# Optimization experiments

Measured on AMD Instinct MI355X. Metric: run time of the kernel, lower is better.

The kernel has to match this reference:

```python
import jax, jax.numpy as jnp
import numpy as np
import math

HID, NH, NKV, HD = 2048, 16, 4, 128
GROUPS = NH // NKV
ROPE_THETA = 10000.0
NBITS = 8


def fake_quant(x, n_bits=NBITS):
    """Per-tensor symmetric min-max fake quantization with STE."""
    qmax = float(2 ** (n_bits - 1) - 1)
    scale = jnp.maximum(jnp.max(jnp.abs(x)) / qmax, jnp.asarray(1e-8, x.dtype))
    q = jnp.clip(jnp.round(x / scale), -qmax - 1.0, qmax) * scale
    return x + jax.lax.stop_gradient(q - x)


def quant_linear(x, w):
    # QuantLinear: fake-quant activation and weight, then x @ w.T
    return jnp.einsum('bsh,oh->bso', fake_quant(x), fake_quant(w))


def rope_cos_sin(position_ids, head_dim, dtype):
    inv_freq = 1.0 / (ROPE_THETA ** (jnp.arange(0, head_dim, 2, dtype=jnp.float32) / head_dim))
    freqs = position_ids.astype(jnp.float32)[..., None] * inv_freq  # [B,S,hd/2]
    emb = jnp.concatenate([freqs, freqs], axis=-1)                   # [B,S,hd]
    return jnp.cos(emb).astype(dtype), jnp.sin(emb).astype(dtype)


def rotate_half(x):
    h = x.shape[-1] // 2
    return jnp.concatenate([-x[..., h:], x[..., :h]], axis=-1)


def setup_inputs() -> dict:
    key = jax.random.key(0)
    ks = jax.random.split(key, 6)
    B, S = 2, 2048
    hidden_states = jax.random.normal(ks[0], (B, S, HID), dtype=jnp.float32)
    neg = jnp.finfo(jnp.float32).min
    causal = jnp.where(jnp.tril(jnp.ones((S, S), dtype=bool)), 0.0, neg).astype(jnp.float32)
    attention_mask = jnp.broadcast_to(causal[None, None], (B, 1, S, S))
    position_ids = jnp.broadcast_to(jnp.arange(S, dtype=jnp.int64)[None], (B, S))
    wq = jax.random.normal(ks[1], (NH * HD, HID), dtype=jnp.float32) * 0.02
    wk = jax.random.normal(ks[2], (NKV * HD, HID), dtype=jnp.float32) * 0.02
    wv = jax.random.normal(ks[3], (NKV * HD, HID), dtype=jnp.float32) * 0.02
    wo = jax.random.normal(ks[4], (HID, NH * HD), dtype=jnp.float32) * 0.02
    return {"hidden_states": hidden_states, "attention_mask": attention_mask,
            "position_ids": position_ids, "wq": wq, "wk": wk, "wv": wv, "wo": wo}


def reference(hidden_states, attention_mask, position_ids, wq, wk, wv, wo):
    B, S, _ = hidden_states.shape
    dtype = hidden_states.dtype
    # quantized projections -> [B, nH, S, hd] / [B, nKV, S, hd]
    q = quant_linear(hidden_states, wq).reshape(B, S, NH, HD).transpose(0, 2, 1, 3)
    k = quant_linear(hidden_states, wk).reshape(B, S, NKV, HD).transpose(0, 2, 1, 3)
    v = quant_linear(hidden_states, wv).reshape(B, S, NKV, HD).transpose(0, 2, 1, 3)
    # RoPE
    cos, sin = rope_cos_sin(position_ids, HD, dtype)
    cos, sin = cos[:, None], sin[:, None]  # broadcast over heads
    q = q * cos + rotate_half(q) * sin
    k = k * cos + rotate_half(k) * sin
    # repeat_kv (GQA)
    k = jnp.repeat(k, GROUPS, axis=1)
    v = jnp.repeat(v, GROUPS, axis=1)
    # fake-quantized QK^T
    q = fake_quant(q)
    k = fake_quant(k)
    attn_weights = jnp.einsum('bhqd,bhkd->bhqk', q, k) / math.sqrt(HD)
    attn_weights = attn_weights + attention_mask
    attn_weights = jnp.maximum(attn_weights, jnp.finfo(attn_weights.dtype).min)
    attn_weights = jax.nn.softmax(attn_weights.astype(jnp.float32), axis=-1).astype(dtype)
    # fake-quantized PV
    p = fake_quant(attn_weights)
    v = fake_quant(v)
    attn_output = jnp.einsum('bhqk,bhkd->bhqd', p, v)
    attn_output = attn_output.transpose(0, 2, 1, 3).reshape(B, S, NH * HD)
    return quant_linear(attn_output, wo)
```

## Files before the change

### kernel.cpp

```cpp
#include <hip/hip_runtime.h>
#include <math.h>
#include <stdint.h>
#include <stddef.h>

#define HID 2048
#define NH 16
#define NKV 4
#define HD 128
#define GROUPS (NH / NKV)
#define BATCH 2
#define SEQ 2048

#define N_HS  8388608ull
#define N_Q   8388608ull
#define N_KV  2097152ull
#define N_WQ  4194304ull
#define N_WKV 1048576ull
#define N_WO  4194304ull

typedef __attribute__((ext_vector_type(8))) short bf16x8;
typedef __attribute__((ext_vector_type(4))) float f32x4;

#define LOG2E 1.4426950408889634f
#define CLAMP_L2 115.41560325f

__device__ inline float quantv(float x, float s) {
  float q = rintf(x / s);
  return fminf(fmaxf(q, -128.0f), 127.0f);
}

__device__ inline float slot_scale(const unsigned int* slots, int i) {
  return fmaxf(__uint_as_float(slots[i]) / 127.0f, 1e-8f);
}

__device__ inline unsigned short f2bf(float x) {
  return (unsigned short)(__float_as_uint(x) >> 16);
}

__device__ inline float amax4(float4 v) {
  return fmaxf(fmaxf(fabsf(v.x), fabsf(v.y)), fmaxf(fabsf(v.z), fabsf(v.w)));
}

__device__ inline void block_amax_atomic(float m, unsigned int* slot) {
  __shared__ float red[256];
  red[threadIdx.x] = m;
  __syncthreads();
  for (int o = 128; o > 0; o >>= 1) {
    if (threadIdx.x < o) red[threadIdx.x] = fmaxf(red[threadIdx.x], red[threadIdx.x + o]);
    __syncthreads();
  }
  if (threadIdx.x == 0) atomicMax(slot, __float_as_uint(red[0]));
}

__device__ __forceinline__ void gload_lds16(const void* g, void* l) {
  __builtin_amdgcn_global_load_lds((const __attribute__((address_space(1))) unsigned int*)g,
                                   (__attribute__((address_space(3))) unsigned int*)l, 16, 0, 0);
}

__global__ __launch_bounds__(256) void absmax5_k(const float* __restrict__ a0,
                                                 const float* __restrict__ a1,
                                                 const float* __restrict__ a2,
                                                 const float* __restrict__ a3,
                                                 const float* __restrict__ a4,
                                                 unsigned int* __restrict__ slots) {
  const int t = blockIdx.y;
  const float* x = t == 0 ? a0 : t == 1 ? a1 : t == 2 ? a2 : t == 3 ? a3 : a4;
  const size_t n4 = (t == 0 ? N_HS : t == 1 ? N_WQ : t == 2 ? N_WKV : t == 3 ? N_WKV : N_WO) / 4;
  const float4* xp = (const float4*)x;
  float m = 0.0f;
  for (size_t i = (size_t)blockIdx.x * 256 + threadIdx.x; i < n4; i += (size_t)gridDim.x * 256)
    m = fmaxf(m, amax4(xp[i]));
  block_amax_atomic(m, slots + t);
}

__global__ __launch_bounds__(256) void quant5_k(const float* __restrict__ a0,
                                                const float* __restrict__ a1,
                                                const float* __restrict__ a2,
                                                const float* __restrict__ a3,
                                                const float* __restrict__ a4,
                                                const unsigned int* __restrict__ slots,
                                                unsigned short* __restrict__ o0,
                                                unsigned short* __restrict__ o1,
                                                unsigned short* __restrict__ o2,
                                                unsigned short* __restrict__ o3,
                                                unsigned short* __restrict__ o4) {
  const int t = blockIdx.y;
  const float* x = t == 0 ? a0 : t == 1 ? a1 : t == 2 ? a2 : t == 3 ? a3 : a4;
  unsigned short* o = t == 0 ? o0 : t == 1 ? o1 : t == 2 ? o2 : t == 3 ? o3 : o4;
  const size_t n4 = (t == 0 ? N_HS : t == 1 ? N_WQ : t == 2 ? N_WKV : t == 3 ? N_WKV : N_WO) / 4;
  const float s = fmaxf(__uint_as_float(slots[t]) / 127.0f, 1e-8f);
  const float4* xp = (const float4*)x;
  ushort4* op = (ushort4*)o;
  for (size_t i = (size_t)blockIdx.x * 256 + threadIdx.x; i < n4; i += (size_t)gridDim.x * 256) {
    float4 v = xp[i];
    ushort4 r;
    r.x = f2bf(quantv(v.x, s));
    r.y = f2bf(quantv(v.y, s));
    r.z = f2bf(quantv(v.z, s));
    r.w = f2bf(quantv(v.w, s));
    op[i] = r;
  }
}

__global__ __launch_bounds__(256) void quant2_k(const float* __restrict__ a0,
                                                const float* __restrict__ a1,
                                                const unsigned int* __restrict__ slots,
                                                unsigned short* __restrict__ o0,
                                                unsigned short* __restrict__ o1) {
  const int t = blockIdx.y;
  const float* x = t == 0 ? a0 : a1;
  unsigned short* o = t == 0 ? o0 : o1;
  const size_t n4 = (t == 0 ? N_Q : N_KV) / 4;
  const float s = fmaxf(__uint_as_float(slots[5 + t]) / 127.0f, 1e-8f);
  const float4* xp = (const float4*)x;
  ushort4* op = (ushort4*)o;
  for (size_t i = (size_t)blockIdx.x * 256 + threadIdx.x; i < n4; i += (size_t)gridDim.x * 256) {
    float4 v = xp[i];
    ushort4 r;
    r.x = f2bf(quantv(v.x, s));
    r.y = f2bf(quantv(v.y, s));
    r.z = f2bf(quantv(v.z, s));
    r.w = f2bf(quantv(v.w, s));
    op[i] = r;
  }
}

__global__ __launch_bounds__(256) void quant1_k(const float* __restrict__ x, size_t n4,
                                                const unsigned int* __restrict__ slot,
                                                unsigned short* __restrict__ out) {
  const float s = fmaxf(__uint_as_float(*slot) / 127.0f, 1e-8f);
  const float4* xp = (const float4*)x;
  ushort4* op = (ushort4*)out;
  for (size_t i = (size_t)blockIdx.x * 256 + threadIdx.x; i < n4; i += (size_t)gridDim.x * 256) {
    float4 v = xp[i];
    ushort4 r;
    r.x = f2bf(quantv(v.x, s));
    r.y = f2bf(quantv(v.y, s));
    r.z = f2bf(quantv(v.z, s));
    r.w = f2bf(quantv(v.w, s));
    op[i] = r;
  }
}

__global__ __launch_bounds__(256) void vtq_k(const float* __restrict__ vbuf,
                                             const unsigned int* __restrict__ slots,
                                             unsigned short* __restrict__ vbt) {
  __shared__ unsigned short L[128 * 72];
  const int tid = threadIdx.x;
  const int s0 = blockIdx.x * 64;
  const int hk = blockIdx.y;
  const int b = blockIdx.z;
  const float s = fmaxf(__uint_as_float(slots[7]) / 127.0f, 1e-8f);
#pragma unroll
  for (int it = 0; it < 8; it++) {
    int idx = tid + it * 256;
    int sl = idx >> 5, c4 = idx & 31;
    float4 v = ((const float4*)(vbuf + ((size_t)(b * SEQ + s0 + sl) * NKV + hk) * HD))[c4];
    L[(c4 * 4 + 0) * 72 + sl] = f2bf(quantv(v.x, s));
    L[(c4 * 4 + 1) * 72 + sl] = f2bf(quantv(v.y, s));
    L[(c4 * 4 + 2) * 72 + sl] = f2bf(quantv(v.z, s));
    L[(c4 * 4 + 3) * 72 + sl] = f2bf(quantv(v.w, s));
  }
  __syncthreads();
  const size_t obase = ((size_t)(b * NKV + hk)) * HD * SEQ + s0;
#pragma unroll
  for (int it = 0; it < 4; it++) {
    int idx = tid + it * 256;
    int d = idx >> 3, sc = idx & 7;
    *(bf16x8*)(vbt + obase + (size_t)d * SEQ + sc * 8) = *(const bf16x8*)(&L[d * 72 + sc * 8]);
  }
}

__device__ __forceinline__ void gemm_body(const unsigned short* __restrict__ A,
                                          const unsigned short* __restrict__ B,
                                          float* __restrict__ C, int N, int K, int m0, int n0,
                                          float sc, int amax_slot, unsigned int* slots) {
  __shared__ unsigned short As[3][128 * 32];
  __shared__ unsigned short Bs[3][128 * 32];
  const int tid = threadIdx.x;
  const int wave = tid >> 6, lane = tid & 63;
  const int l16 = lane & 15, quad = lane >> 4;
  const int wm = (wave & 1) * 64, wn = (wave >> 1) * 64;

  f32x4 acc[4][4];
#pragma unroll
  for (int i = 0; i < 4; i++)
#pragma unroll
    for (int j = 0; j < 4; j++) acc[i][j] = (f32x4){0.f, 0.f, 0.f, 0.f};

  auto STAGE = [&](int buf, int kt) {
#pragma unroll
    for (int it = 0; it < 2; it++) {
      int c = it * 256 + tid;
      int r = c >> 2, kc = (c & 3) * 8;
      gload_lds16(A + (size_t)(m0 + r) * K + kt + kc, &As[buf][(it * 256 + wave * 64) * 8]);
      gload_lds16(B + (size_t)(n0 + r) * K + kt + kc, &Bs[buf][(it * 256 + wave * 64) * 8]);
    }
  };

  const int nk = K / 32;
  STAGE(0, 0);
  STAGE(1, 32);
  STAGE(2, 64);
  for (int t = 0; t < nk; t++) {
    const int buf = t % 3;
    if (t + 3 < nk + 1)      asm volatile("s_waitcnt vmcnt(8)" ::: "memory");
    else if (t + 2 < nk + 1) asm volatile("s_waitcnt vmcnt(4)" ::: "memory");
    else                     asm volatile("s_waitcnt vmcnt(0)" ::: "memory");
    __builtin_amdgcn_sched_barrier(0);
    __builtin_amdgcn_s_barrier();
    __builtin_amdgcn_sched_barrier(0);
    bf16x8 af[4], bq[4];
#pragma unroll
    for (int i = 0; i < 4; i++)
      af[i] = *(const bf16x8*)(&As[buf][(wm + i * 16 + l16) * 32 + quad * 8]);
#pragma unroll
    for (int j = 0; j < 4; j++)
      bq[j] = *(const bf16x8*)(&Bs[buf][(wn + j * 16 + l16) * 32 + quad * 8]);
    asm volatile("s_waitcnt lgkmcnt(0)" ::: "memory");
    __builtin_amdgcn_sched_barrier(0);
    __builtin_amdgcn_s_barrier();
    __builtin_amdgcn_sched_barrier(0);
    if (t + 3 < nk) STAGE(buf, (t + 3) * 32);
#pragma unroll
    for (int i = 0; i < 4; i++)
#pragma unroll
      for (int j = 0; j < 4; j++)
        acc[i][j] = __builtin_amdgcn_mfma_f32_16x16x32_bf16(af[i], bq[j], acc[i][j], 0, 0, 0);
  }

  float am = 0.0f;
#pragma unroll
  for (int i = 0; i < 4; i++)
#pragma unroll
    for (int j = 0; j < 4; j++)
#pragma unroll
      for (int r = 0; r < 4; r++) {
        int row = m0 + wm + i * 16 + quad * 4 + r;
        int col = n0 + wn + j * 16 + l16;
        float v = acc[i][j][r] * sc;
        C[(size_t)row * N + col] = v;
        am = fmaxf(am, fabsf(v));
      }
  if (amax_slot >= 0) {
    __syncthreads();
    float* red = (float*)As;
    red[tid] = am;
    __syncthreads();
    for (int o = 128; o > 0; o >>= 1) {
      if (tid < o) red[tid] = fmaxf(red[tid], red[tid + o]);
      __syncthreads();
    }
    if (tid == 0) atomicMax(slots + amax_slot, __float_as_uint(red[0]));
  }
}

__global__ __launch_bounds__(256) void gemm_qkv_k(const unsigned short* __restrict__ A,
                                                  const unsigned short* __restrict__ Bq,
                                                  const unsigned short* __restrict__ Bk,
                                                  const unsigned short* __restrict__ Bv,
                                                  float* __restrict__ Cq, float* __restrict__ Ck,
                                                  float* __restrict__ Cv,
                                                  unsigned int* __restrict__ slots) {
  const int nt = blockIdx.x, m0 = blockIdx.y * 128;
  const unsigned short* B;
  float* C;
  int N, n0, ib, amx;
  if (nt < 16) {
    B = Bq; C = Cq; N = 2048; n0 = nt * 128; ib = 1; amx = -1;
  } else if (nt < 20) {
    B = Bk; C = Ck; N = 512; n0 = (nt - 16) * 128; ib = 2; amx = -1;
  } else {
    B = Bv; C = Cv; N = 512; n0 = (nt - 20) * 128; ib = 3; amx = 7;
  }
  const float sc = slot_scale(slots, 0) * slot_scale(slots, ib);
  gemm_body(A, B, C, N, HID, m0, n0, sc, amx, slots);
}

__global__ __launch_bounds__(256) void gemm_o_k(const unsigned short* __restrict__ A,
                                                const unsigned short* __restrict__ B,
                                                float* __restrict__ C,
                                                unsigned int* __restrict__ slots) {
  const float sc = slot_scale(slots, 8) * slot_scale(slots, 4);
  gemm_body(A, B, C, HID, NH * HD, blockIdx.y * 128, blockIdx.x * 128, sc, -1, slots);
}

__global__ __launch_bounds__(256) void rope_table_k(float2* __restrict__ tab) {
  int idx = blockIdx.x * 256 + threadIdx.x;
  int i = idx & 63, s = idx >> 6;
  float inv = 1.0f / powf(10000.0f, (float)(2 * i) * (1.0f / 128.0f));
  float fr = (float)s * inv;
  tab[idx] = make_float2(cosf(fr), sinf(fr));
}

__global__ __launch_bounds__(256) void rope_kernel(float* __restrict__ t, int nh, int nhs,
                                                   const float2* __restrict__ tab,
                                                   unsigned int* __restrict__ slot) {
  const size_t total4 = (size_t)BATCH * SEQ * nh * 16;
  float am = 0.0f;
  for (size_t it = (size_t)blockIdx.x * 256 + threadIdx.x; it < total4;
       it += (size_t)gridDim.x * 256) {
    const int i4 = (int)(it & 15);
    const int h = (int)((it >> 4) & (nh - 1));
    const int s = (int)((it >> (4 + nhs)) & (SEQ - 1));
    const int b = (int)(it >> (15 + nhs));
    const size_t base = ((size_t)(b * SEQ + s) * nh + h) * HD + i4 * 4;
    float4 x1 = *(const float4*)(t + base);
    float4 x2 = *(const float4*)(t + base + 64);
    const float4* tp = (const float4*)(tab + (s << 6) + i4 * 4);
    float4 cs01 = tp[0];
    float4 cs23 = tp[1];
    float4 r1, r2;
    r1.x = x1.x * cs01.x - x2.x * cs01.y;  r2.x = x2.x * cs01.x + x1.x * cs01.y;
    r1.y = x1.y * cs01.z - x2.y * cs01.w;  r2.y = x2.y * cs01.z + x1.y * cs01.w;
    r1.z = x1.z * cs23.x - x2.z * cs23.y;  r2.z = x2.z * cs23.x + x1.z * cs23.y;
    r1.w = x1.w * cs23.z - x2.w * cs23.w;  r2.w = x2.w * cs23.z + x1.w * cs23.w;
    *(float4*)(t + base) = r1;
    *(float4*)(t + base + 64) = r2;
    am = fmaxf(am, fmaxf(amax4(r1), amax4(r2)));
  }
  block_amax_atomic(am, slot);
}

#define TK 64
#define KS_STRIDE (HD + 8)
#define VT_STRIDE (TK + 8)
#define PS_STRIDE (TK + 8)

__device__ __forceinline__ void ldK(bf16x8 r[4], const unsigned short* kb, int b, int hk,
                                    int j0, int tid) {
#pragma unroll
  for (int it = 0; it < 4; it++) {
    int c2 = tid + it * 256;
    int rr = c2 >> 4, c = c2 & 15;
    r[it] = *(const bf16x8*)(kb + ((size_t)(b * SEQ + j0 + rr) * NKV + hk) * HD + c * 8);
  }
}
__device__ __forceinline__ void stK(unsigned short* Ks, const bf16x8 r[4], int tid) {
#pragma unroll
  for (int it = 0; it < 4; it++) {
    int c2 = tid + it * 256;
    int rr = c2 >> 4, c = c2 & 15;
    *(bf16x8*)(&Ks[rr * KS_STRIDE + c * 8]) = r[it];
  }
}
__device__ __forceinline__ void ldV(bf16x8 r[4], const unsigned short* vbt, size_t vbase,
                                    int j0, int tid) {
#pragma unroll
  for (int it = 0; it < 4; it++) {
    int idx = tid + it * 256;
    int d = idx >> 3, sc = idx & 7;
    r[it] = *(const bf16x8*)(vbt + vbase + (size_t)d * SEQ + j0 + sc * 8);
  }
}
__device__ __forceinline__ void stV(unsigned short* Vt, const bf16x8 r[4], int tid) {
#pragma unroll
  for (int it = 0; it < 4; it++) {
    int idx = tid + it * 256;
    int d = idx >> 3, sc = idx & 7;
    *(bf16x8*)(&Vt[d * VT_STRIDE + sc * 8]) = r[it];
  }
}

__device__ __forceinline__ void qk41(f32x4 sfr[4], const unsigned short* Ks,
                                     const bf16x8 qf[4], int l16, int quad) {
#pragma unroll
  for (int kt = 0; kt < 4; kt++) {
    f32x4 a = {0.f, 0.f, 0.f, 0.f};
    const unsigned short* kp = &Ks[(kt * 16 + l16) * KS_STRIDE + quad * 8];
#pragma unroll
    for (int s = 0; s < 4; s++)
      a = __builtin_amdgcn_mfma_f32_16x16x32_bf16(*(const bf16x8*)(kp + s * 32), qf[s], a,
                                                  0, 0, 0);
    sfr[kt] = a;
  }
}
__device__ __forceinline__ void lacc(float& l, const f32x4 sfr[4], float c1, bool diag,
                                     int j0, int qrow, int quad) {
  if (!diag) {
#pragma unroll
    for (int kt = 0; kt < 4; kt++)
#pragma unroll
      for (int r = 0; r < 4; r++)
        l += __builtin_amdgcn_exp2f(fminf(sfr[kt][r] * c1, CLAMP_L2));
  } else {
#pragma unroll
    for (int kt = 0; kt < 4; kt++) {
      const int key0 = j0 + kt * 16 + quad * 4;
#pragma unroll
      for (int r = 0; r < 4; r++) {
        float e = __builtin_amdgcn_exp2f(fminf(sfr[kt][r] * c1, CLAMP_L2));
        l += (key0 + r <= qrow) ? e : 0.0f;
      }
    }
  }
}
__device__ __forceinline__ void pquant(unsigned short* Psb, const f32x4 sfr[4],
                                       float l2il, float c1, bool diag, int j0,
                                       int qrow, int wave, int l16, int quad) {
  unsigned short* rowp = &Psb[(wave * 16 + l16) * PS_STRIDE + quad * 4];
#pragma unroll
  for (int kt = 0; kt < 4; kt++) {
    const int key0 = j0 + kt * 16 + quad * 4;
    float p0 = rintf(__builtin_amdgcn_exp2f(fminf(sfr[kt][0] * c1, CLAMP_L2) + l2il));
    float p1 = rintf(__builtin_amdgcn_exp2f(fminf(sfr[kt][1] * c1, CLAMP_L2) + l2il));
    float p2 = rintf(__builtin_amdgcn_exp2f(fminf(sfr[kt][2] * c1, CLAMP_L2) + l2il));
    float p3 = rintf(__builtin_amdgcn_exp2f(fminf(sfr[kt][3] * c1, CLAMP_L2) + l2il));
    if (diag) {
      if (key0 + 0 > qrow) p0 = 0.0f;
      if (key0 + 1 > qrow) p1 = 0.0f;
      if (key0 + 2 > qrow) p2 = 0.0f;
      if (key0 + 3 > qrow) p3 = 0.0f;
    }
    ushort4 pk;
    pk.x = f2bf(p0);
    pk.y = f2bf(p1);
    pk.z = f2bf(p2);
    pk.w = f2bf(p3);
    *(ushort4*)(rowp + kt * 16) = pk;
  }
}
__device__ __forceinline__ void pvacc1(f32x4 of[8], const unsigned short* Ps,
                                       const unsigned short* Vt, int wave, int l16, int quad) {
  const unsigned short* pp = &Ps[(wave * 16 + l16) * PS_STRIDE + quad * 8];
  bf16x8 p0 = *(const bf16x8*)pp;
  bf16x8 p1 = *(const bf16x8*)(pp + 32);
#pragma unroll
  for (int n = 0; n < 8; n++) {
    const unsigned short* vp = &Vt[(n * 16 + l16) * VT_STRIDE + quad * 8];
    of[n] = __builtin_amdgcn_mfma_f32_16x16x32_bf16(p0, *(const bf16x8*)vp, of[n], 0, 0, 0);
    of[n] = __builtin_amdgcn_mfma_f32_16x16x32_bf16(p1, *(const bf16x8*)(vp + 32), of[n],
                                                    0, 0, 0);
  }
}

__global__ __launch_bounds__(256, 3) void attn_mfma_kernel(const unsigned short* __restrict__ qb,
                                                           const unsigned short* __restrict__ kb,
                                                           const unsigned short* __restrict__ vbt,
                                                           float* __restrict__ ob,
                                                           unsigned int* __restrict__ slots) {
  __shared__ unsigned short Ks[TK * KS_STRIDE];
  __shared__ unsigned short Vt[HD * VT_STRIDE];
  __shared__ unsigned short Ps[64 * PS_STRIDE];

  const int tid = threadIdx.x;
  const int wave = tid >> 6;
  const int lane = tid & 63;
  const int l16 = lane & 15;
  const int quad = lane >> 4;
  const int id = blockIdx.x;
  const int b = (id & 7) >> 2;
  const int hk = id & 3;
  const int j = id >> 3;
  const int h = hk * GROUPS + (j & 3);
  const int tile = 31 - (j >> 2);
  const int q0 = tile * 64, nt = tile + 1;

  const float s_q = slot_scale(slots, 5);
  const float s_k = slot_scale(slots, 6);
  const float s_v = slot_scale(slots, 7);
  const float ss = s_q * s_k / 11.313708498984761f;
  const float c1 = ss * LOG2E;
  const float scale_p = 1.0f / 127.0f;
  const size_t vbase = ((size_t)(b * NKV + hk)) * HD * SEQ;

  bf16x8 qf[4];
  {
    const unsigned short* qp =
        qb + ((size_t)(b * SEQ + q0 + wave * 16 + l16) * NH + h) * HD + quad * 8;
#pragma unroll
    for (int s = 0; s < 4; s++) qf[s] = *(const bf16x8*)(qp + s * 32);
  }
  const int qrow = q0 + wave * 16 + l16;
  const int qrb = q0 + wave * 16 + quad * 4;

  float l = 0.f;
  bf16x8 kreg[4];
  ldK(kreg, kb, b, hk, 0, tid);
  for (int t = 0; t < nt; t++) {
    const int j0 = t * TK;
    __syncthreads();
    stK(Ks, kreg, tid);
    if (t + 1 < nt) ldK(kreg, kb, b, hk, (t + 1) * TK, tid);
    __syncthreads();
    f32x4 sfr[4];
    qk41(sfr, Ks, qf, l16, quad);
    lacc(l, sfr, c1, t == nt - 1, j0, qrow, quad);
  }
  l += __shfl_xor(l, 16);
  l += __shfl_xor(l, 32);
  const float l2il = __log2f(127.0f / fmaxf(l, 1e-30f));

  f32x4 of[8];
#pragma unroll
  for (int n = 0; n < 8; n++) of[n] = (f32x4){0.f, 0.f, 0.f, 0.f};
  bf16x8 vreg[4];
  ldK(kreg, kb, b, hk, 0, tid);
  ldV(vreg, vbt, vbase, 0, tid);
  for (int t = 0; t < nt; t++) {
    const int j0 = t * TK;
    __syncthreads();
    stK(Ks, kreg, tid);
    stV(Vt, vreg, tid);
    if (t + 1 < nt) {
      ldK(kreg, kb, b, hk, (t + 1) * TK, tid);
      ldV(vreg, vbt, vbase, (t + 1) * TK, tid);
    }
    __syncthreads();
    f32x4 sfr[4];
    qk41(sfr, Ks, qf, l16, quad);
    pquant(Ps, sfr, l2il, c1, t == nt - 1, j0, qrow, wave, l16, quad);
    pvacc1(of, Ps, Vt, wave, l16, quad);
  }

  const float oscale = scale_p * s_v;
  float amax = 0.0f;
#pragma unroll
  for (int n = 0; n < 8; n++)
#pragma unroll
    for (int r = 0; r < 4; r++) {
      float v = of[n][r] * oscale;
      ob[((size_t)(b * SEQ + qrb + r) * NH + h) * HD + n * 16 + l16] = v;
      amax = fmaxf(amax, fabsf(v));
    }
  __syncthreads();
  float* red = (float*)Ps;
  red[tid] = amax;
  __syncthreads();
  for (int o = 128; o > 0; o >>= 1) {
    if (tid < o) red[tid] = fmaxf(red[tid], red[tid + o]);
    __syncthreads();
  }
  if (tid == 0) atomicMax(slots + 8, __float_as_uint(red[0]));
}

extern "C" void kernel_launch(void* const* d_in, const int* in_sizes, int n_in,
                              void* d_out, int out_size, void* d_ws, size_t ws_size,
                              hipStream_t stream) {
  const float* hs = (const float*)d_in[0];
  const float* wq = (const float*)d_in[3];
  const float* wk = (const float*)d_in[4];
  const float* wv = (const float*)d_in[5];
  const float* wo = (const float*)d_in[6];
  float* out = (float*)d_out;

  unsigned int* slots = (unsigned int*)d_ws;
  char* p = (char*)d_ws + 256;
  unsigned short* hsq = (unsigned short*)p;  p += 2 * N_HS;
  unsigned short* wqq = (unsigned short*)p;  p += 2 * N_WQ;
  unsigned short* wkq = (unsigned short*)p;  p += 2 * N_WKV;
  unsigned short* wvq = (unsigned short*)p;  p += 2 * N_WKV;
  unsigned short* woq = (unsigned short*)p;  p += 2 * N_WO;
  float* kbuf = (float*)p;                   p += 4 * N_KV;
  float* vbuf = (float*)p;                   p += 4 * N_KV;
  unsigned short* qbf = (unsigned short*)p;  p += 2 * N_Q;
  unsigned short* kbf = (unsigned short*)p;  p += 2 * N_KV;
  unsigned short* vbt = (unsigned short*)p;  p += 2 * N_KV;
  float2* rtab = (float2*)p;
  unsigned short* aobf = hsq;
  float* qbuf = out;
  float* aobuf = out;

  hipMemsetAsync(d_ws, 0, 256, stream);

  rope_table_k<<<(SEQ * 64) / 256, 256, 0, stream>>>(rtab);
  absmax5_k<<<dim3(256, 5), 256, 0, stream>>>(hs, wq, wk, wv, wo, slots);
  quant5_k<<<dim3(256, 5), 256, 0, stream>>>(hs, wq, wk, wv, wo, slots, hsq, wqq, wkq, wvq, woq);

  const int M = BATCH * SEQ;
  gemm_qkv_k<<<dim3(24, M / 128), 256, 0, stream>>>(hsq, wqq, wkq, wvq, qbuf, kbuf, vbuf, slots);

  rope_kernel<<<1024, 256, 0, stream>>>(qbuf, NH, 4, rtab, slots + 5);
  rope_kernel<<<256, 256, 0, stream>>>(kbuf, NKV, 2, rtab, slots + 6);

  quant2_k<<<dim3(256, 2), 256, 0, stream>>>(qbuf, kbuf, slots, qbf, kbf);
  vtq_k<<<dim3(SEQ / 64, NKV, BATCH), 256, 0, stream>>>(vbuf, slots, vbt);

  attn_mfma_kernel<<<dim3(1024, 1, 1), 256, 0, stream>>>(qbf, kbf, vbt, aobuf, slots);

  quant1_k<<<256, 256, 0, stream>>>(aobuf, N_Q / 4, slots + 8, aobf);

  gemm_o_k<<<dim3(HID / 128, M / 128), 256, 0, stream>>>(aobf, woq, out, slots);
}
```

Baseline: 412.7 us.

## Swap QK work split so each wave owns a key slice across all query rows

Each wave now keeps Q fragments for all 64 query rows of the block in registers and loads only its own 16-key slice of K from LDS once per tile. Before, every wave reread all 64 keys of the tile for its own 16 query rows. This cuts LDS reads of K by a factor of four. The row sums of the softmax denominator are now split across waves and must be combined through LDS with an extra barrier. The P tile is likewise written cooperatively, so the PV step needs another __syncthreads per tile. Holding 16 Q fragments raises register pressure, which could hurt occupancy under launch_bounds(256,3).

Measured after the change: 472.7 us. 1.15x slower.

```diff
diff --git a/kernel.cpp b/kernel.cpp
--- a/kernel.cpp
+++ b/kernel.cpp
@@ -362,63 +362,18 @@
   }
 }
 
-__device__ __forceinline__ void qk41(f32x4 sfr[4], const unsigned short* Ks,
-                                     const bf16x8 qf[4], int l16, int quad) {
-#pragma unroll
-  for (int kt = 0; kt < 4; kt++) {
-    f32x4 a = {0.f, 0.f, 0.f, 0.f};
-    const unsigned short* kp = &Ks[(kt * 16 + l16) * KS_STRIDE + quad * 8];
-#pragma unroll
-    for (int s = 0; s < 4; s++)
-      a = __builtin_amdgcn_mfma_f32_16x16x32_bf16(*(const bf16x8*)(kp + s * 32), qf[s], a,
-                                                  0, 0, 0);
-    sfr[kt] = a;
-  }
-}
-__device__ __forceinline__ void lacc(float& l, const f32x4 sfr[4], float c1, bool diag,
-                                     int j0, int qrow, int quad) {
-  if (!diag) {
-#pragma unroll
-    for (int kt = 0; kt < 4; kt++)
-#pragma unroll
-      for (int r = 0; r < 4; r++)
-        l += __builtin_amdgcn_exp2f(fminf(sfr[kt][r] * c1, CLAMP_L2));
-  } else {
-#pragma unroll
-    for (int kt = 0; kt < 4; kt++) {
-      const int key0 = j0 + kt * 16 + quad * 4;
-#pragma unroll
-      for (int r = 0; r < 4; r++) {
-        float e = __builtin_amdgcn_exp2f(fminf(sfr[kt][r] * c1, CLAMP_L2));
-        l += (key0 + r <= qrow) ? e : 0.0f;
-      }
-    }
-  }
-}
-__device__ __forceinline__ void pquant(unsigned short* Psb, const f32x4 sfr[4],
-                                       float l2il, float c1, bool diag, int j0,
-                                       int qrow, int wave, int l16, int quad) {
-  unsigned short* rowp = &Psb[(wave * 16 + l16) * PS_STRIDE + quad * 4];
-#pragma unroll
-  for (int kt = 0; kt < 4; kt++) {
-    const int key0 = j0 + kt * 16 + quad * 4;
-    float p0 = rintf(__builtin_amdgcn_exp2f(fminf(sfr[kt][0] * c1, CLAMP_L2) + l2il));
-    float p1 = rintf(__builtin_amdgcn_exp2f(fminf(sfr[kt][1] * c1, CLAMP_L2) + l2il));
-    float p2 = rintf(__builtin_amdgcn_exp2f(fminf(sfr[kt][2] * c1, CLAMP_L2) + l2il));
-    float p3 = rintf(__builtin_amdgcn_exp2f(fminf(sfr[kt][3] * c1, CLAMP_L2) + l2il));
-    if (diag) {
-      if (key0 + 0 > qrow) p0 = 0.0f;
-      if (key0 + 1 > qrow) p1 = 0.0f;
-      if (key0 + 2 > qrow) p2 = 0.0f;
-      if (key0 + 3 > qrow) p3 = 0.0f;
-    }
-    ushort4 pk;
-    pk.x = f2bf(p0);
-    pk.y = f2bf(p1);
-    pk.z = f2bf(p2);
-    pk.w = f2bf(p3);
-    *(ushort4*)(rowp + kt * 16) = pk;
-  }
+__device__ __forceinline__ void ldKf(bf16x8 kf[4], const unsigned short* Ks, int wave,
+                                     int l16, int quad) {
+  const unsigned short* kp = &Ks[(wave * 16 + l16) * KS_STRIDE + quad * 8];
+#pragma unroll
+  for (int s = 0; s < 4; s++) kf[s] = *(const bf16x8*)(kp + s * 32);
+}
+__device__ __forceinline__ f32x4 qk_g(const bf16x8 kf[4], const bf16x8* qfg) {
+  f32x4 a = {0.f, 0.f, 0.f, 0.f};
+#pragma unroll
+  for (int s = 0; s < 4; s++)
+    a = __builtin_amdgcn_mfma_f32_16x16x32_bf16(kf[s], qfg[s], a, 0, 0, 0);
+  return a;
 }
 __device__ __forceinline__ void pvacc1(f32x4 of[8], const unsigned short* Ps,
                                        const unsigned short* Vt, int wave, int l16, int quad) {
@@ -464,32 +419,64 @@
   const float scale_p = 1.0f / 127.0f;
   const size_t vbase = ((size_t)(b * NKV + hk)) * HD * SEQ;
 
-  bf16x8 qf[4];
-  {
+  bf16x8 qf[16];
+#pragma unroll
+  for (int g = 0; g < 4; g++) {
     const unsigned short* qp =
-        qb + ((size_t)(b * SEQ + q0 + wave * 16 + l16) * NH + h) * HD + quad * 8;
-#pragma unroll
-    for (int s = 0; s < 4; s++) qf[s] = *(const bf16x8*)(qp + s * 32);
-  }
-  const int qrow = q0 + wave * 16 + l16;
+        qb + ((size_t)(b * SEQ + q0 + g * 16 + l16) * NH + h) * HD + quad * 8;
+#pragma unroll
+    for (int s = 0; s < 4; s++) qf[g * 4 + s] = *(const bf16x8*)(qp + s * 32);
+  }
   const int qrb = q0 + wave * 16 + quad * 4;
 
-  float l = 0.f;
+  float l[4] = {0.f, 0.f, 0.f, 0.f};
   bf16x8 kreg[4];
   ldK(kreg, kb, b, hk, 0, tid);
   for (int t = 0; t < nt; t++) {
-    const int j0 = t * TK;
     __syncthreads();
     stK(Ks, kreg, tid);
     if (t + 1 < nt) ldK(kreg, kb, b, hk, (t + 1) * TK, tid);
     __syncthreads();
-    f32x4 sfr[4];
-    qk41(sfr, Ks, qf, l16, quad);
-    lacc(l, sfr, c1, t == nt - 1, j0, qrow, quad);
-  }
-  l += __shfl_xor(l, 16);
-  l += __shfl_xor(l, 32);
-  const float l2il = __log2f(127.0f / fmaxf(l, 1e-30f));
+    bf16x8 kf[4];
+    ldKf(kf, Ks, wave, l16, quad);
+    const bool diag = (t == nt - 1);
+    const int key0 = t * TK + wave * 16 + quad * 4;
+#pragma unroll
+    for (int g = 0; g < 4; g++) {
+      f32x4 a = qk_g(kf, &qf[g * 4]);
+      if (!diag) {
+#pragma unroll
+        for (int r = 0; r < 4; r++)
+          l[g] += __builtin_amdgcn_exp2f(fminf(a[r] * c1, CLAMP_L2));
+      } else {
+        const int qrow = q0 + g * 16 + l16;
+#pragma unroll
+        for (int r = 0; r < 4; r++) {
+          float e = __builtin_amdgcn_exp2f(fminf(a[r] * c1, CLAMP_L2));
+          l[g] += (key0 + r <= qrow) ? e : 0.0f;
+        }
+      }
+    }
+  }
+#pragma unroll
+  for (int g = 0; g < 4; g++) {
+    l[g] += __shfl_xor(l[g], 16);
+    l[g] += __shfl_xor(l[g], 32);
+  }
+  {
+    float* Lr = (float*)Ps;
+    if (quad == 0) {
+#pragma unroll
+      for (int g = 0; g < 4; g++) Lr[wave * 64 + g * 16 + l16] = l[g];
+    }
+    __syncthreads();
+#pragma unroll
+    for (int g = 0; g < 4; g++) {
+      float s = Lr[g * 16 + l16] + Lr[64 + g * 16 + l16] + Lr[128 + g * 16 + l16] +
+                Lr[192 + g * 16 + l16];
+      l[g] = __log2f(127.0f / fmaxf(s, 1e-30f));
+    }
+  }
 
   f32x4 of[8];
 #pragma unroll
@@ -498,7 +485,6 @@
   ldK(kreg, kb, b, hk, 0, tid);
   ldV(vreg, vbt, vbase, 0, tid);
   for (int t = 0; t < nt; t++) {
-    const int j0 = t * TK;
     __syncthreads();
     stK(Ks, kreg, tid);
     stV(Vt, vreg, tid);
@@ -507,9 +493,32 @@
       ldV(vreg, vbt, vbase, (t + 1) * TK, tid);
     }
     __syncthreads();
-    f32x4 sfr[4];
-    qk41(sfr, Ks, qf, l16, quad);
-    pquant(Ps, sfr, l2il, c1, t == nt - 1, j0, qrow, wave, l16, quad);
+    bf16x8 kf[4];
+    ldKf(kf, Ks, wave, l16, quad);
+    const bool diag = (t == nt - 1);
+    const int key0 = t * TK + wave * 16 + quad * 4;
+#pragma unroll
+    for (int g = 0; g < 4; g++) {
+      f32x4 a = qk_g(kf, &qf[g * 4]);
+      float p0 = rintf(__builtin_amdgcn_exp2f(fminf(a[0] * c1, CLAMP_L2) + l[g]));
+      float p1 = rintf(__builtin_amdgcn_exp2f(fminf(a[1] * c1, CLAMP_L2) + l[g]));
+      float p2 = rintf(__builtin_amdgcn_exp2f(fminf(a[2] * c1, CLAMP_L2) + l[g]));
+      float p3 = rintf(__builtin_amdgcn_exp2f(fminf(a[3] * c1, CLAMP_L2) + l[g]));
+      if (diag) {
+        const int qrow = q0 + g * 16 + l16;
+        if (key0 + 0 > qrow) p0 = 0.0f;
+        if (key0 + 1 > qrow) p1 = 0.0f;
+        if (key0 + 2 > qrow) p2 = 0.0f;
+        if (key0 + 3 > qrow) p3 = 0.0f;
+      }
+      ushort4 pk;
+      pk.x = f2bf(p0);
+      pk.y = f2bf(p1);
+      pk.z = f2bf(p2);
+      pk.w = f2bf(p3);
+      *(ushort4*)(&Ps[(g * 16 + l16) * PS_STRIDE + wave * 16 + quad * 4]) = pk;
+    }
+    __syncthreads();
     pvacc1(of, Ps, Vt, wave, l16, quad);
   }
 
```
